# Kernel tuning notes

Hardware: AMD Instinct MI355X
Metric: run time of the kernel (lower is better)

The kernel has to match this reference:

```python
import jax, jax.numpy as jnp
import numpy as np

B, T, C = 8, 2048, 1024
HEAD = 128
ROPE_BASE = 10000.0


def _rope_cos_sin(T, head_dim, base=ROPE_BASE):
    half = head_dim // 2
    inv_freq = base ** (-jnp.arange(half, dtype=jnp.float32) / half)  # (half,)
    t = jnp.arange(T, dtype=jnp.float32)[:, None]                    # (T,1)
    freqs = t * inv_freq[None, :]                                    # (T, half)
    return jnp.cos(freqs), jnp.sin(freqs)


def apply_rope(x, cos, sin):
    # x: (B,T,D), cos/sin: (T,D/2); pairwise (interleaved) rotation
    x_even = x[..., ::2]
    x_odd = x[..., 1::2]
    c = cos[None]
    s = sin[None]
    r_even = x_even * c - x_odd * s
    r_odd = x_even * s + x_odd * c
    # interleave back: (..., D/2, 2) -> (..., D)
    return jnp.stack([r_even, r_odd], axis=-1).reshape(x.shape)


def setup_inputs() -> dict:
    key = jax.random.key(0)
    kx, kk, kq, kv = jax.random.split(key, 4)
    x = jax.random.normal(kx, (B, T, C), dtype=jnp.float32)
    # nn.Linear default init scale ~ 1/sqrt(fan_in); keep activations sane
    scale = 1.0 / np.sqrt(C)
    Wk = jax.random.normal(kk, (C, HEAD), dtype=jnp.float32) * scale
    Wq = jax.random.normal(kq, (C, HEAD), dtype=jnp.float32) * scale
    Wv = jax.random.normal(kv, (C, HEAD), dtype=jnp.float32) * scale
    cos, sin = _rope_cos_sin(T, HEAD)
    return {"x": x, "cos": cos, "sin": sin, "Wk": Wk, "Wq": Wq, "Wv": Wv}


def reference(x, cos, sin, Wk, Wq, Wv):
    # QKV projections (no bias, per nn.Linear(..., bias=False))
    k = jnp.einsum('btc,cd->btd', x, Wk)
    q = jnp.einsum('btc,cd->btd', x, Wq)
    v = jnp.einsum('btc,cd->btd', x, Wv)
    q = apply_rope(q, cos, sin)
    k = apply_rope(k, cos, sin)
    d = k.shape[-1]
    wei = jnp.einsum('bqd,bkd->bqk', q, k) / jnp.sqrt(jnp.asarray(d, q.dtype))
    t = x.shape[1]
    causal = jnp.tril(jnp.ones((t, t), dtype=bool))
    wei = jnp.where(causal[None], wei, jnp.asarray(-jnp.inf, wei.dtype))
    wei = jax.nn.softmax(wei, axis=-1)
    # dropout is identity in eval/reference mode
    out = jnp.einsum('bqk,bkd->bqd', wei, v)
    return out
```

## Files before the change

### kernel.cpp

```cpp
#include <hip/hip_runtime.h>

#define B_ 8
#define T_ 2048
#define C_ 1024
#define D_ 128
#define M_ (B_*T_)

typedef __attribute__((ext_vector_type(4))) float f32x4;
typedef __attribute__((ext_vector_type(8))) short s16x8;

static __device__ __forceinline__ ushort f2bf(float f){
  unsigned u = __float_as_uint(f);
  u = (u + 0x7fffu + ((u >> 16) & 1u)) >> 16;
  return (ushort)u;
}
static __device__ __forceinline__ float bf2f(ushort u){
  return __uint_as_float(((unsigned)u) << 16);
}
static __device__ __forceinline__ unsigned cvt_pk_bf16(float lo, float hi){
  unsigned r;
  asm volatile("v_cvt_pk_bf16_f32 %0, %1, %2" : "=v"(r) : "v"(lo), "v"(hi));
  return r;
}

__global__ __launch_bounds__(256) void prep_kernel(
    const float* __restrict__ x,
    const float* __restrict__ Wk, const float* __restrict__ Wq, const float* __restrict__ Wv,
    ushort* __restrict__ xbf, ushort* __restrict__ wt)
{
  int bid = blockIdx.x, tid = threadIdx.x;
  if (bid < 8192) {
    int idx = bid * 256 + tid;
    const float4* xp = (const float4*)x;
    float4 a = xp[idx * 2], b = xp[idx * 2 + 1];
    uint4 st;
    st.x = (unsigned)f2bf(a.x) | ((unsigned)f2bf(a.y) << 16);
    st.y = (unsigned)f2bf(a.z) | ((unsigned)f2bf(a.w) << 16);
    st.z = (unsigned)f2bf(b.x) | ((unsigned)f2bf(b.y) << 16);
    st.w = (unsigned)f2bf(b.z) | ((unsigned)f2bf(b.w) << 16);
    ((uint4*)xbf)[idx] = st;
  } else {
    int j = (bid - 8192) * 256 + tid;
    if (j < 384 * 1024) {
      int n3 = j >> 10, k = j & 1023;
      int sel = n3 >> 7, n = n3 & 127;
      const float* W = (sel == 0) ? Wq : (sel == 1) ? Wk : Wv;
      wt[j] = f2bf(W[k * 128 + n]);
    }
  }
}

__global__ __launch_bounds__(512) void qkv_kernel(
    const ushort* __restrict__ xbf, const ushort* __restrict__ wt,
    const float* __restrict__ cosp, const float* __restrict__ sinp,
    ushort* __restrict__ Qw, ushort* __restrict__ Kw, ushort* __restrict__ VT)
{
  __shared__ __align__(16) ushort As[2][64 * 64];
  __shared__ __align__(16) ushort Bs[2][384 * 64];
  const int tid = threadIdx.x;
  const int m0  = blockIdx.x * 64;
  const int wid = tid >> 6, lane = tid & 63;
  const int wm = wid >> 2, wn = wid & 3;
  const int g = lane >> 4, l15 = lane & 15;

  f32x4 acc[2][6];
  #pragma unroll
  for (int i = 0; i < 2; i++)
    #pragma unroll
    for (int j = 0; j < 6; j++) acc[i][j] = f32x4{0.f, 0.f, 0.f, 0.f};

  const int o = tid * 16;
  const int srow = o >> 7;
  const int scb  = (o & 127) ^ ((srow & 7) << 4);
  const char* xbase = (const char*)xbf + (size_t)(m0 + srow) * 2048 + scb;
  const char* wbase = (const char*)wt + (size_t)srow * 2048 + scb;

  auto stage = [&](int k0, int bb) {
    __builtin_amdgcn_global_load_lds(
        (const __attribute__((address_space(1))) void*)(xbase + k0 * 2),
        (__attribute__((address_space(3))) void*)((char*)As + bb * 8192 + o), 16, 0, 0);
    #pragma unroll
    for (int j = 0; j < 6; j++) {
      __builtin_amdgcn_global_load_lds(
          (const __attribute__((address_space(1))) void*)(wbase + (size_t)j * 64 * 2048 + k0 * 2),
          (__attribute__((address_space(3))) void*)((char*)Bs + bb * 49152 + j * 8192 + o), 16, 0, 0);
    }
  };

  stage(0, 0);
  __syncthreads();
  int bb = 0;
  for (int k0 = 0; k0 < 1024; k0 += 64) {
    if (k0 + 64 < 1024) stage(k0 + 64, bb ^ 1);
    const char* Ab = (const char*)As + bb * 8192;
    const char* Bb = (const char*)Bs + bb * 49152;
    #pragma unroll
    for (int kk = 0; kk < 2; kk++) {
      s16x8 af[2];
      #pragma unroll
      for (int mi = 0; mi < 2; mi++) {
        int row = wm * 32 + mi * 16 + l15;
        int cb  = (kk * 64 + g * 16) ^ ((row & 7) << 4);
        af[mi] = *(const s16x8*)(Ab + row * 128 + cb);
      }
      s16x8 bfr[6];
      #pragma unroll
      for (int n = 0; n < 6; n++) {
        int col = wn * 96 + n * 16 + l15;
        int cb2 = (kk * 64 + g * 16) ^ ((col & 7) << 4);
        bfr[n] = *(const s16x8*)(Bb + col * 128 + cb2);
      }
      __builtin_amdgcn_s_setprio(1);
      #pragma unroll
      for (int mi = 0; mi < 2; mi++)
        #pragma unroll
        for (int n = 0; n < 6; n++)
          acc[mi][n] = __builtin_amdgcn_mfma_f32_16x16x32_bf16(af[mi], bfr[n], acc[mi][n], 0, 0, 0);
      __builtin_amdgcn_s_setprio(0);
    }
    __syncthreads();
    bb ^= 1;
  }

  const int rowb0 = m0 + wm * 32;
  #pragma unroll
  for (int mi = 0; mi < 2; mi++) {
    #pragma unroll
    for (int n = 0; n < 6; n++) {
      int colbase = wn * 96 + n * 16;
      int region  = colbase >> 7;
      int dcol    = (colbase & 127) + l15;
      int rowb    = rowb0 + mi * 16 + g * 4;
      if (region < 2) {
        ushort* dst = region ? Kw : Qw;
        int ii = dcol >> 1;
        float sgn = (dcol & 1) ? 1.0f : -1.0f;
        #pragma unroll
        for (int r = 0; r < 4; r++) {
          float own  = acc[mi][n][r];
          float part = __shfl_xor(own, 1, 64);
          int row = rowb + r;
          int t   = row & 2047;
          float c = cosp[t * 64 + ii], s = sinp[t * 64 + ii];
          float val = own * c + sgn * part * s;
          dst[row * 128 + dcol] = f2bf(val);
        }
      } else {
        int t0 = rowb & 2047;
        int b  = rowb >> 11;
        unsigned w0 = (unsigned)f2bf(acc[mi][n][0]) | ((unsigned)f2bf(acc[mi][n][1]) << 16);
        unsigned w1 = (unsigned)f2bf(acc[mi][n][2]) | ((unsigned)f2bf(acc[mi][n][3]) << 16);
        uint2 st; st.x = w0; st.y = w1;
        *(uint2*)(VT + (size_t)b * (128 * 2048) + dcol * 2048 + t0) = st;
      }
    }
  }
}

__global__ __launch_bounds__(256) void attn_kernel(
    const ushort* __restrict__ Qw, const ushort* __restrict__ Kw,
    const ushort* __restrict__ VT, ushort* __restrict__ Opart,
    float* __restrict__ Ml)
{
  __shared__ __align__(16) ushort KVs[2][16384];
  const int tid = threadIdx.x;
  const int w = tid >> 6, lane = tid & 63;
  const int g = lane >> 4, l15 = lane & 15;

  const int bid = blockIdx.x;
  const int b   = bid / 144;
  const int idx = bid - b * 144;
  int a = 0;
  #pragma unroll
  for (int t = 1; t < 8; t++) if (idx >= 2 * t * (t + 1)) a = t;
  const int rem = idx - 2 * a * (a + 1);
  const int jin = rem / (a + 1);
  const int c   = rem - jin * (a + 1);
  const int j   = a * 4 + jin;
  const int q0  = j * 64;
  const int kv_base = c * 256;
  const int kv_end  = min(kv_base + 256, q0 + 64);
  const int nt  = (kv_end - kv_base) >> 6;
  const int qg  = q0 + w * 16 + l15;

  const ushort* Qb = Qw + (size_t)b * T_ * 128;
  const char* Kbase = (const char*)(Kw + (size_t)b * T_ * 128);
  const char* Vbase = (const char*)(VT + (size_t)b * 128 * T_);

  auto stage = [&](int kv0, int bbuf) {
    char* Kd = (char*)&KVs[bbuf][0];
    char* Vd = (char*)&KVs[bbuf][8192];
    #pragma unroll
    for (int p = 0; p < 4; p++) {
      int oo = p * 4096 + tid * 16;
      int r = oo >> 8, cin = oo & 255;
      int cb = cin ^ ((r & 7) << 4);
      __builtin_amdgcn_global_load_lds(
          (const __attribute__((address_space(1))) void*)(Kbase + (size_t)(kv0 + r) * 256 + cb),
          (__attribute__((address_space(3))) void*)(Kd + oo), 16, 0, 0);
    }
    #pragma unroll
    for (int p = 0; p < 4; p++) {
      int oo = p * 4096 + tid * 16;
      int r = oo >> 7, cin = oo & 127;
      int cb = cin ^ ((r & 7) << 4);
      __builtin_amdgcn_global_load_lds(
          (const __attribute__((address_space(1))) void*)(Vbase + (size_t)r * 4096 + (size_t)kv0 * 2 + cb),
          (__attribute__((address_space(3))) void*)(Vd + oo), 16, 0, 0);
    }
  };

  s16x8 qf[4];
  #pragma unroll
  for (int kd = 0; kd < 4; kd++)
    qf[kd] = *(const s16x8*)(Qb + qg * 128 + kd * 32 + g * 8);

  f32x4 acco[8];
  #pragma unroll
  for (int i = 0; i < 8; i++) acco[i] = f32x4{0.f, 0.f, 0.f, 0.f};
  float mrun = -1e30f, lrun = 0.0f;
  const float scale = 0.08838834764831845f;

  stage(kv_base, 0);
  __syncthreads();
  int bbuf = 0;
  for (int t = 0; t < nt; t++) {
    int kv0 = kv_base + t * 64;
    if (t + 1 < nt) stage(kv0 + 64, bbuf ^ 1);
    const char* Kd = (const char*)&KVs[bbuf][0];
    const char* Vd = (const char*)&KVs[bbuf][8192];

    f32x4 accs[4];
    #pragma unroll
    for (int h = 0; h < 4; h++) accs[h] = f32x4{0.f, 0.f, 0.f, 0.f};
    __builtin_amdgcn_s_setprio(1);
    #pragma unroll
    for (int h = 0; h < 4; h++) {
      int rr = h * 16 + l15;
      int rs = rr * 256;
      int sw = (rr & 7) << 4;
      #pragma unroll
      for (int kd = 0; kd < 4; kd++) {
        s16x8 kf = *(const s16x8*)(Kd + rs + ((kd * 64 + g * 16) ^ sw));
        accs[h] = __builtin_amdgcn_mfma_f32_16x16x32_bf16(kf, qf[kd], accs[h], 0, 0, 0);
      }
    }
    __builtin_amdgcn_s_setprio(0);

    float p[4][4];
    float pmax = -1e30f;
    #pragma unroll
    for (int h = 0; h < 4; h++)
      #pragma unroll
      for (int r = 0; r < 4; r++) {
        int kvg = kv0 + h * 16 + g * 4 + r;
        float sv = accs[h][r] * scale;
        sv = (kvg <= qg) ? sv : -1e30f;
        p[h][r] = sv;
        pmax = fmaxf(pmax, sv);
      }
    pmax = fmaxf(pmax, __shfl_xor(pmax, 16, 64));
    pmax = fmaxf(pmax, __shfl_xor(pmax, 32, 64));
    float mnew = fmaxf(mrun, pmax);
    float f = __expf(mrun - mnew);
    float psum = 0.0f;
    #pragma unroll
    for (int h = 0; h < 4; h++)
      #pragma unroll
      for (int r = 0; r < 4; r++) { float e = __expf(p[h][r] - mnew); p[h][r] = e; psum += e; }
    psum += __shfl_xor(psum, 16, 64);
    psum += __shfl_xor(psum, 32, 64);
    lrun = lrun * f + psum;
    mrun = mnew;
    #pragma unroll
    for (int i = 0; i < 8; i++) acco[i] *= f;

    unsigned pbw[2][4];
    #pragma unroll
    for (int hk = 0; hk < 2; hk++) {
      unsigned v0 = cvt_pk_bf16(p[2 * hk][0], p[2 * hk][1]);
      unsigned v1 = cvt_pk_bf16(p[2 * hk][2], p[2 * hk][3]);
      unsigned v2 = cvt_pk_bf16(p[2 * hk + 1][0], p[2 * hk + 1][1]);
      unsigned v3 = cvt_pk_bf16(p[2 * hk + 1][2], p[2 * hk + 1][3]);
      #pragma unroll
      for (int wd = 0; wd < 4; wd++) {
        int src = (((g & 1) * 2 + (wd >> 1)) << 4) + l15;
        unsigned t0 = __shfl((wd & 1) ? v1 : v0, src, 64);
        unsigned t1 = __shfl((wd & 1) ? v3 : v2, src, 64);
        pbw[hk][wd] = (g < 2) ? t0 : t1;
      }
    }
    s16x8 pbv0 = *(s16x8*)pbw[0];
    s16x8 pbv1 = *(s16x8*)pbw[1];

    __builtin_amdgcn_s_setprio(1);
    #pragma unroll
    for (int dt = 0; dt < 8; dt++) {
      int rr = dt * 16 + l15;
      int rs = rr * 128;
      int sw = (rr & 7) << 4;
      s16x8 vf0 = *(const s16x8*)(Vd + rs + ((g * 16) ^ sw));
      s16x8 vf1 = *(const s16x8*)(Vd + rs + ((64 + g * 16) ^ sw));
      acco[dt] = __builtin_amdgcn_mfma_f32_16x16x32_bf16(vf0, pbv0, acco[dt], 0, 0, 0);
      acco[dt] = __builtin_amdgcn_mfma_f32_16x16x32_bf16(vf1, pbv1, acco[dt], 0, 0, 0);
    }
    __builtin_amdgcn_s_setprio(0);
    __syncthreads();
    bbuf ^= 1;
  }

  float inv = 1.0f / lrun;
  ushort* ob = Opart + (size_t)bid * 8192 + (w * 16 + l15) * 128;
  #pragma unroll
  for (int dt = 0; dt < 8; dt++) {
    f32x4 o4 = acco[dt] * inv;
    uint2 st;
    st.x = cvt_pk_bf16(o4[0], o4[1]);
    st.y = cvt_pk_bf16(o4[2], o4[3]);
    *(uint2*)(ob + dt * 16 + g * 4) = st;
  }
  if (lane < 16) {
    Ml[(size_t)bid * 128 + (w * 16 + lane) * 2]     = mrun;
    Ml[(size_t)bid * 128 + (w * 16 + lane) * 2 + 1] = lrun;
  }
}

__global__ __launch_bounds__(512) void combine_kernel(
    const ushort* __restrict__ Opart, const float* __restrict__ Ml,
    float* __restrict__ out)
{
  const int bq = blockIdx.x;
  const int b = bq >> 5, j = bq & 31;
  const int a = j >> 2, jin = j & 3, nch = a + 1;
  const int s0 = b * 144 + 2 * a * (a + 1) + jin * (a + 1);
  const int tid = threadIdx.x;
  const int row = tid >> 3, ci = tid & 7;

  float M = -1e30f;
  for (int c = 0; c < nch; c++)
    M = fmaxf(M, Ml[(size_t)(s0 + c) * 128 + row * 2]);

  float acc[16];
  #pragma unroll
  for (int k = 0; k < 16; k++) acc[k] = 0.f;
  float W = 0.f;
  for (int c = 0; c < nch; c++) {
    float m = Ml[(size_t)(s0 + c) * 128 + row * 2];
    float l = Ml[(size_t)(s0 + c) * 128 + row * 2 + 1];
    float wgt = l * __expf(m - M);
    W += wgt;
    const ushort* vp = Opart + (size_t)(s0 + c) * 8192 + row * 128 + ci * 16;
    s16x8 v0 = *(const s16x8*)vp;
    s16x8 v1 = *(const s16x8*)(vp + 8);
    #pragma unroll
    for (int k = 0; k < 8; k++) {
      acc[k]     += wgt * bf2f((ushort)v0[k]);
      acc[8 + k] += wgt * bf2f((ushort)v1[k]);
    }
  }
  float invW = 1.0f / W;
  float* op = out + ((size_t)(b * 2048 + j * 64 + row)) * 128 + ci * 16;
  #pragma unroll
  for (int q = 0; q < 4; q++) {
    f32x4 o4 { acc[q*4]*invW, acc[q*4+1]*invW, acc[q*4+2]*invW, acc[q*4+3]*invW };
    *(f32x4*)(op + q * 4) = o4;
  }
}

extern "C" void kernel_launch(void* const* d_in, const int* in_sizes, int n_in,
                              void* d_out, int out_size, void* d_ws, size_t ws_size,
                              hipStream_t stream)
{
  const float* x    = (const float*)d_in[0];
  const float* cosp = (const float*)d_in[1];
  const float* sinp = (const float*)d_in[2];
  const float* Wk   = (const float*)d_in[3];
  const float* Wq   = (const float*)d_in[4];
  const float* Wv   = (const float*)d_in[5];
  char* ws = (char*)d_ws;
  ushort* xbf   = (ushort*)ws;
  ushort* wt    = (ushort*)(ws + 33554432);
  ushort* Qw    = (ushort*)(ws + 34340864);
  ushort* Kw    = (ushort*)(ws + 38535168);
  ushort* VT    = (ushort*)(ws + 42729472);
  ushort* Opart = (ushort*)ws;
  float*  Ml    = (float*)(ws + 18874368);
  float* outp = (float*)d_out;

  prep_kernel<<<9728, 256, 0, stream>>>(x, Wk, Wq, Wv, xbf, wt);
  qkv_kernel<<<256, 512, 0, stream>>>(xbf, wt, cosp, sinp, Qw, Kw, VT);
  attn_kernel<<<1152, 256, 0, stream>>>(Qw, Kw, VT, Opart, Ml);
  combine_kernel<<<256, 512, 0, stream>>>(Opart, Ml, outp);
}
```

Measured before the change: 175.6 us.

## Fuse x bf16 conversion into QKV GEMM and double attention query tile

Removes the separate full-x fp32-to-bf16 conversion pass: the QKV GEMM now loads fp32 x directly, converts it in registers and writes the bf16 tile into LDS while the B tile streams in asynchronously. The attention kernel now handles 128 query rows per block (two 16-row subtiles per wave), so each K/V tile staged in LDS is reused twice. This halves the number of attention blocks and split partials, at the cost of more registers per wave and possibly lower occupancy. The workspace layout and the combine indexing are updated to match.

Measured after the change: 167.7 us. -4.5%, faster.

```diff
diff --git a/kernel.cpp b/kernel.cpp
--- a/kernel.cpp
+++ b/kernel.cpp
@@ -4,7 +4,6 @@
 #define T_ 2048
 #define C_ 1024
 #define D_ 128
-#define M_ (B_*T_)
 
 typedef __attribute__((ext_vector_type(4))) float f32x4;
 typedef __attribute__((ext_vector_type(8))) short s16x8;
@@ -23,35 +22,19 @@
   return r;
 }
 
-__global__ __launch_bounds__(256) void prep_kernel(
-    const float* __restrict__ x,
+__global__ __launch_bounds__(256) void wprep_kernel(
     const float* __restrict__ Wk, const float* __restrict__ Wq, const float* __restrict__ Wv,
-    ushort* __restrict__ xbf, ushort* __restrict__ wt)
+    ushort* __restrict__ wt)
 {
-  int bid = blockIdx.x, tid = threadIdx.x;
-  if (bid < 8192) {
-    int idx = bid * 256 + tid;
-    const float4* xp = (const float4*)x;
-    float4 a = xp[idx * 2], b = xp[idx * 2 + 1];
-    uint4 st;
-    st.x = (unsigned)f2bf(a.x) | ((unsigned)f2bf(a.y) << 16);
-    st.y = (unsigned)f2bf(a.z) | ((unsigned)f2bf(a.w) << 16);
-    st.z = (unsigned)f2bf(b.x) | ((unsigned)f2bf(b.y) << 16);
-    st.w = (unsigned)f2bf(b.z) | ((unsigned)f2bf(b.w) << 16);
-    ((uint4*)xbf)[idx] = st;
-  } else {
-    int j = (bid - 8192) * 256 + tid;
-    if (j < 384 * 1024) {
-      int n3 = j >> 10, k = j & 1023;
-      int sel = n3 >> 7, n = n3 & 127;
-      const float* W = (sel == 0) ? Wq : (sel == 1) ? Wk : Wv;
-      wt[j] = f2bf(W[k * 128 + n]);
-    }
-  }
+  int j = blockIdx.x * 256 + threadIdx.x;
+  int n3 = j >> 10, k = j & 1023;
+  int sel = n3 >> 7, n = n3 & 127;
+  const float* W = (sel == 0) ? Wq : (sel == 1) ? Wk : Wv;
+  wt[j] = f2bf(W[k * 128 + n]);
 }
 
 __global__ __launch_bounds__(512) void qkv_kernel(
-    const ushort* __restrict__ xbf, const ushort* __restrict__ wt,
+    const float* __restrict__ x, const ushort* __restrict__ wt,
     const float* __restrict__ cosp, const float* __restrict__ sinp,
     ushort* __restrict__ Qw, ushort* __restrict__ Kw, ushort* __restrict__ VT)
 {
@@ -72,13 +55,13 @@
   const int o = tid * 16;
   const int srow = o >> 7;
   const int scb  = (o & 127) ^ ((srow & 7) << 4);
-  const char* xbase = (const char*)xbf + (size_t)(m0 + srow) * 2048 + scb;
   const char* wbase = (const char*)wt + (size_t)srow * 2048 + scb;
-
-  auto stage = [&](int k0, int bb) {
-    __builtin_amdgcn_global_load_lds(
-        (const __attribute__((address_space(1))) void*)(xbase + k0 * 2),
-        (__attribute__((address_space(3))) void*)((char*)As + bb * 8192 + o), 16, 0, 0);
+  const int arow = tid >> 3;
+  const int ac8  = (tid & 7) * 8;
+  const float* xp = x + (size_t)(m0 + arow) * 1024 + ac8;
+  const int adst = arow * 64 + (((tid & 7) * 8) ^ ((arow & 7) << 3));
+
+  auto stageB = [&](int k0, int bb) {
     #pragma unroll
     for (int j = 0; j < 6; j++) {
       __builtin_amdgcn_global_load_lds(
@@ -86,12 +69,29 @@
           (__attribute__((address_space(3))) void*)((char*)Bs + bb * 49152 + j * 8192 + o), 16, 0, 0);
     }
   };
-
-  stage(0, 0);
+  auto writeA = [&](f32x4 a0, f32x4 a1, int bb) {
+    unsigned aw[4];
+    aw[0] = cvt_pk_bf16(a0[0], a0[1]);
+    aw[1] = cvt_pk_bf16(a0[2], a0[3]);
+    aw[2] = cvt_pk_bf16(a1[0], a1[1]);
+    aw[3] = cvt_pk_bf16(a1[2], a1[3]);
+    *(s16x8*)(&As[bb][adst]) = *(s16x8*)aw;
+  };
+
+  {
+    f32x4 a0 = *(const f32x4*)(xp);
+    f32x4 a1 = *(const f32x4*)(xp + 4);
+    stageB(0, 0);
+    writeA(a0, a1, 0);
+  }
   __syncthreads();
   int bb = 0;
   for (int k0 = 0; k0 < 1024; k0 += 64) {
-    if (k0 + 64 < 1024) stage(k0 + 64, bb ^ 1);
+    int k1 = (k0 + 64 < 1024) ? k0 + 64 : 0;
+    f32x4 n0 = *(const f32x4*)(xp + k1);
+    f32x4 n1 = *(const f32x4*)(xp + k1 + 4);
+    stageB(k1, bb ^ 1);
+
     const char* Ab = (const char*)As + bb * 8192;
     const char* Bb = (const char*)Bs + bb * 49152;
     #pragma unroll
@@ -118,6 +118,7 @@
           acc[mi][n] = __builtin_amdgcn_mfma_f32_16x16x32_bf16(af[mi], bfr[n], acc[mi][n], 0, 0, 0);
       __builtin_amdgcn_s_setprio(0);
     }
+    writeA(n0, n1, bb ^ 1);
     __syncthreads();
     bb ^= 1;
   }
@@ -168,20 +169,22 @@
   const int g = lane >> 4, l15 = lane & 15;
 
   const int bid = blockIdx.x;
-  const int b   = bid / 144;
-  const int idx = bid - b * 144;
+  const int b   = bid / 72;
+  const int idx = bid - b * 72;
   int a = 0;
   #pragma unroll
-  for (int t = 1; t < 8; t++) if (idx >= 2 * t * (t + 1)) a = t;
-  const int rem = idx - 2 * a * (a + 1);
+  for (int t = 1; t < 8; t++) if (idx >= t * (t + 1)) a = t;
+  const int rem = idx - a * (a + 1);
   const int jin = rem / (a + 1);
   const int c   = rem - jin * (a + 1);
-  const int j   = a * 4 + jin;
-  const int q0  = j * 64;
+  const int j   = 2 * a + jin;
+  const int q0  = j * 128;
   const int kv_base = c * 256;
-  const int kv_end  = min(kv_base + 256, q0 + 64);
+  const int kv_end  = min(kv_base + 256, q0 + 128);
   const int nt  = (kv_end - kv_base) >> 6;
-  const int qg  = q0 + w * 16 + l15;
+  int qg[2];
+  qg[0] = q0 + w * 32 + l15;
+  qg[1] = qg[0] + 16;
 
   const ushort* Qb = Qw + (size_t)b * T_ * 128;
   const char* Kbase = (const char*)(Kw + (size_t)b * T_ * 128);
@@ -210,15 +213,19 @@
     }
   };
 
-  s16x8 qf[4];
-  #pragma unroll
-  for (int kd = 0; kd < 4; kd++)
-    qf[kd] = *(const s16x8*)(Qb + qg * 128 + kd * 32 + g * 8);
-
-  f32x4 acco[8];
-  #pragma unroll
-  for (int i = 0; i < 8; i++) acco[i] = f32x4{0.f, 0.f, 0.f, 0.f};
-  float mrun = -1e30f, lrun = 0.0f;
+  s16x8 qf[2][4];
+  #pragma unroll
+  for (int i = 0; i < 2; i++)
+    #pragma unroll
+    for (int kd = 0; kd < 4; kd++)
+      qf[i][kd] = *(const s16x8*)(Qb + (size_t)qg[i] * 128 + kd * 32 + g * 8);
+
+  f32x4 acco[2][8];
+  #pragma unroll
+  for (int i = 0; i < 2; i++)
+    #pragma unroll
+    for (int d = 0; d < 8; d++) acco[i][d] = f32x4{0.f, 0.f, 0.f, 0.f};
+  float mrun[2] = {-1e30f, -1e30f}, lrun[2] = {0.f, 0.f};
   const float scale = 0.08838834764831845f;
 
   stage(kv_base, 0);
@@ -230,9 +237,11 @@
     const char* Kd = (const char*)&KVs[bbuf][0];
     const char* Vd = (const char*)&KVs[bbuf][8192];
 
-    f32x4 accs[4];
-    #pragma unroll
-    for (int h = 0; h < 4; h++) accs[h] = f32x4{0.f, 0.f, 0.f, 0.f};
+    f32x4 accs[2][4];
+    #pragma unroll
+    for (int i = 0; i < 2; i++)
+      #pragma unroll
+      for (int h = 0; h < 4; h++) accs[i][h] = f32x4{0.f, 0.f, 0.f, 0.f};
     __builtin_amdgcn_s_setprio(1);
     #pragma unroll
     for (int h = 0; h < 4; h++) {
@@ -242,56 +251,60 @@
       #pragma unroll
       for (int kd = 0; kd < 4; kd++) {
         s16x8 kf = *(const s16x8*)(Kd + rs + ((kd * 64 + g * 16) ^ sw));
-        accs[h] = __builtin_amdgcn_mfma_f32_16x16x32_bf16(kf, qf[kd], accs[h], 0, 0, 0);
+        accs[0][h] = __builtin_amdgcn_mfma_f32_16x16x32_bf16(kf, qf[0][kd], accs[0][h], 0, 0, 0);
+        accs[1][h] = __builtin_amdgcn_mfma_f32_16x16x32_bf16(kf, qf[1][kd], accs[1][h], 0, 0, 0);
       }
     }
     __builtin_amdgcn_s_setprio(0);
 
-    float p[4][4];
-    float pmax = -1e30f;
-    #pragma unroll
-    for (int h = 0; h < 4; h++)
-      #pragma unroll
-      for (int r = 0; r < 4; r++) {
-        int kvg = kv0 + h * 16 + g * 4 + r;
-        float sv = accs[h][r] * scale;
-        sv = (kvg <= qg) ? sv : -1e30f;
-        p[h][r] = sv;
-        pmax = fmaxf(pmax, sv);
+    s16x8 pbv[2][2];
+    #pragma unroll
+    for (int i = 0; i < 2; i++) {
+      float p[4][4];
+      float pmax = -1e30f;
+      #pragma unroll
+      for (int h = 0; h < 4; h++)
+        #pragma unroll
+        for (int r = 0; r < 4; r++) {
+          int kvg = kv0 + h * 16 + g * 4 + r;
+          float sv = accs[i][h][r] * scale;
+          sv = (kvg <= qg[i]) ? sv : -1e30f;
+          p[h][r] = sv;
+          pmax = fmaxf(pmax, sv);
+        }
+      pmax = fmaxf(pmax, __shfl_xor(pmax, 16, 64));
+      pmax = fmaxf(pmax, __shfl_xor(pmax, 32, 64));
+      float mnew = fmaxf(mrun[i], pmax);
+      float f = __expf(mrun[i] - mnew);
+      float psum = 0.0f;
+      #pragma unroll
+      for (int h = 0; h < 4; h++)
+        #pragma unroll
+        for (int r = 0; r < 4; r++) { float e = __expf(p[h][r] - mnew); p[h][r] = e; psum += e; }
+      psum += __shfl_xor(psum, 16, 64);
+      psum += __shfl_xor(psum, 32, 64);
+      lrun[i] = lrun[i] * f + psum;
+      mrun[i] = mnew;
+      #pragma unroll
+      for (int d = 0; d < 8; d++) acco[i][d] *= f;
+
+      #pragma unroll
+      for (int hk = 0; hk < 2; hk++) {
+        unsigned v0 = cvt_pk_bf16(p[2 * hk][0], p[2 * hk][1]);
+        unsigned v1 = cvt_pk_bf16(p[2 * hk][2], p[2 * hk][3]);
+        unsigned v2 = cvt_pk_bf16(p[2 * hk + 1][0], p[2 * hk + 1][1]);
+        unsigned v3 = cvt_pk_bf16(p[2 * hk + 1][2], p[2 * hk + 1][3]);
+        unsigned pb[4];
+        #pragma unroll
+        for (int wd = 0; wd < 4; wd++) {
+          int src = (((g & 1) * 2 + (wd >> 1)) << 4) + l15;
+          unsigned t0 = __shfl((wd & 1) ? v1 : v0, src, 64);
+          unsigned t1 = __shfl((wd & 1) ? v3 : v2, src, 64);
+          pb[wd] = (g < 2) ? t0 : t1;
+        }
+        pbv[i][hk] = *(s16x8*)pb;
       }
-    pmax = fmaxf(pmax, __shfl_xor(pmax, 16, 64));
-    pmax = fmaxf(pmax, __shfl_xor(pmax, 32, 64));
-    float mnew = fmaxf(mrun, pmax);
-    float f = __expf(mrun - mnew);
-    float psum = 0.0f;
-    #pragma unroll
-    for (int h = 0; h < 4; h++)
-      #pragma unroll
-      for (int r = 0; r < 4; r++) { float e = __expf(p[h][r] - mnew); p[h][r] = e; psum += e; }
-    psum += __shfl_xor(psum, 16, 64);
-    psum += __shfl_xor(psum, 32, 64);
-    lrun = lrun * f + psum;
-    mrun = mnew;
-    #pragma unroll
-    for (int i = 0; i < 8; i++) acco[i] *= f;
-
-    unsigned pbw[2][4];
-    #pragma unroll
-    for (int hk = 0; hk < 2; hk++) {
-      unsigned v0 = cvt_pk_bf16(p[2 * hk][0], p[2 * hk][1]);
-      unsigned v1 = cvt_pk_bf16(p[2 * hk][2], p[2 * hk][3]);
-      unsigned v2 = cvt_pk_bf16(p[2 * hk + 1][0], p[2 * hk + 1][1]);
-      unsigned v3 = cvt_pk_bf16(p[2 * hk + 1][2], p[2 * hk + 1][3]);
-      #pragma unroll
-      for (int wd = 0; wd < 4; wd++) {
-        int src = (((g & 1) * 2 + (wd >> 1)) << 4) + l15;
-        unsigned t0 = __shfl((wd & 1) ? v1 : v0, src, 64);
-        unsigned t1 = __shfl((wd & 1) ? v3 : v2, src, 64);
-        pbw[hk][wd] = (g < 2) ? t0 : t1;
-      }
-    }
-    s16x8 pbv0 = *(s16x8*)pbw[0];
-    s16x8 pbv1 = *(s16x8*)pbw[1];
+    }
 
     __builtin_amdgcn_s_setprio(1);
     #pragma unroll
@@ -301,27 +314,32 @@
       int sw = (rr & 7) << 4;
       s16x8 vf0 = *(const s16x8*)(Vd + rs + ((g * 16) ^ sw));
       s16x8 vf1 = *(const s16x8*)(Vd + rs + ((64 + g * 16) ^ sw));
-      acco[dt] = __builtin_amdgcn_mfma_f32_16x16x32_bf16(vf0, pbv0, acco[dt], 0, 0, 0);
-      acco[dt] = __builtin_amdgcn_mfma_f32_16x16x32_bf16(vf1, pbv1, acco[dt], 0, 0, 0);
+      acco[0][dt] = __builtin_amdgcn_mfma_f32_16x16x32_bf16(vf0, pbv[0][0], acco[0][dt], 0, 0, 0);
+      acco[0][dt] = __builtin_amdgcn_mfma_f32_16x16x32_bf16(vf1, pbv[0][1], acco[0][dt], 0, 0, 0);
+      acco[1][dt] = __builtin_amdgcn_mfma_f32_16x16x32_bf16(vf0, pbv[1][0], acco[1][dt], 0, 0, 0);
+      acco[1][dt] = __builtin_amdgcn_mfma_f32_16x16x32_bf16(vf1, pbv[1][1], acco[1][dt], 0, 0, 0);
     }
     __builtin_amdgcn_s_setprio(0);
     __syncthreads();
     bbuf ^= 1;
   }
 
-  float inv = 1.0f / lrun;
-  ushort* ob = Opart + (size_t)bid * 8192 + (w * 16 + l15) * 128;
-  #pragma unroll
-  for (int dt = 0; dt < 8; dt++) {
-    f32x4 o4 = acco[dt] * inv;
-    uint2 st;
-    st.x = cvt_pk_bf16(o4[0], o4[1]);
-    st.y = cvt_pk_bf16(o4[2], o4[3]);
-    *(uint2*)(ob + dt * 16 + g * 4) = st;
-  }
-  if (lane < 16) {
-    Ml[(size_t)bid * 128 + (w * 16 + lane) * 2]     = mrun;
-    Ml[(size_t)bid * 128 + (w * 16 + lane) * 2 + 1] = lrun;
+  #pragma unroll
+  for (int i = 0; i < 2; i++) {
+    float inv = 1.0f / lrun[i];
+    ushort* ob = Opart + (size_t)bid * 16384 + (w * 32 + i * 16 + l15) * 128;
+    #pragma unroll
+    for (int dt = 0; dt < 8; dt++) {
+      f32x4 o4 = acco[i][dt] * inv;
+      uint2 st;
+      st.x = cvt_pk_bf16(o4[0], o4[1]);
+      st.y = cvt_pk_bf16(o4[2], o4[3]);
+      *(uint2*)(ob + dt * 16 + g * 4) = st;
+    }
+    if (lane < 16) {
+      Ml[(size_t)bid * 256 + (w * 32 + i * 16 + lane) * 2]     = mrun[i];
+      Ml[(size_t)bid * 256 + (w * 32 + i * 16 + lane) * 2 + 1] = lrun[i];
+    }
   }
 }
 
@@ -330,26 +348,27 @@
     float* __restrict__ out)
 {
   const int bq = blockIdx.x;
-  const int b = bq >> 5, j = bq & 31;
-  const int a = j >> 2, jin = j & 3, nch = a + 1;
-  const int s0 = b * 144 + 2 * a * (a + 1) + jin * (a + 1);
+  const int b = bq >> 5, h = bq & 31;
+  const int j = h >> 1, half = h & 1;
+  const int a = j >> 1, jin = j & 1, nch = a + 1;
+  const int s0 = b * 72 + a * (a + 1) + jin * (a + 1);
   const int tid = threadIdx.x;
-  const int row = tid >> 3, ci = tid & 7;
+  const int row = half * 64 + (tid >> 3), ci = tid & 7;
 
   float M = -1e30f;
   for (int c = 0; c < nch; c++)
-    M = fmaxf(M, Ml[(size_t)(s0 + c) * 128 + row * 2]);
+    M = fmaxf(M, Ml[(size_t)(s0 + c) * 256 + row * 2]);
 
   float acc[16];
   #pragma unroll
   for (int k = 0; k < 16; k++) acc[k] = 0.f;
   float W = 0.f;
   for (int c = 0; c < nch; c++) {
-    float m = Ml[(size_t)(s0 + c) * 128 + row * 2];
-    float l = Ml[(size_t)(s0 + c) * 128 + row * 2 + 1];
+    float m = Ml[(size_t)(s0 + c) * 256 + row * 2];
+    float l = Ml[(size_t)(s0 + c) * 256 + row * 2 + 1];
     float wgt = l * __expf(m - M);
     W += wgt;
-    const ushort* vp = Opart + (size_t)(s0 + c) * 8192 + row * 128 + ci * 16;
+    const ushort* vp = Opart + (size_t)(s0 + c) * 16384 + row * 128 + ci * 16;
     s16x8 v0 = *(const s16x8*)vp;
     s16x8 v1 = *(const s16x8*)(vp + 8);
     #pragma unroll
@@ -359,7 +378,7 @@
     }
   }
   float invW = 1.0f / W;
-  float* op = out + ((size_t)(b * 2048 + j * 64 + row)) * 128 + ci * 16;
+  float* op = out + ((size_t)(b * 2048 + h * 64 + (tid >> 3))) * 128 + ci * 16;
   #pragma unroll
   for (int q = 0; q < 4; q++) {
     f32x4 o4 { acc[q*4]*invW, acc[q*4+1]*invW, acc[q*4+2]*invW, acc[q*4+3]*invW };
@@ -378,17 +397,16 @@
   const float* Wq   = (const float*)d_in[4];
   const float* Wv   = (const float*)d_in[5];
   char* ws = (char*)d_ws;
-  ushort* xbf   = (ushort*)ws;
-  ushort* wt    = (ushort*)(ws + 33554432);
-  ushort* Qw    = (ushort*)(ws + 34340864);
-  ushort* Kw    = (ushort*)(ws + 38535168);
-  ushort* VT    = (ushort*)(ws + 42729472);
-  ushort* Opart = (ushort*)ws;
-  float*  Ml    = (float*)(ws + 18874368);
+  ushort* wt    = (ushort*)ws;
+  ushort* Qw    = (ushort*)(ws + 1048576);
+  ushort* Kw    = (ushort*)(ws + 5242880);
+  ushort* VT    = (ushort*)(ws + 9437184);
+  ushort* Opart = (ushort*)(ws + 13631488);
+  float*  Ml    = (float*)(ws + 32505856);
   float* outp = (float*)d_out;
 
-  prep_kernel<<<9728, 256, 0, stream>>>(x, Wk, Wq, Wv, xbf, wt);
-  qkv_kernel<<<256, 512, 0, stream>>>(xbf, wt, cosp, sinp, Qw, Kw, VT);
-  attn_kernel<<<1152, 256, 0, stream>>>(Qw, Kw, VT, Opart, Ml);
+  wprep_kernel<<<1536, 256, 0, stream>>>(Wk, Wq, Wv, wt);
+  qkv_kernel<<<256, 512, 0, stream>>>(x, wt, cosp, sinp, Qw, Kw, VT);
+  attn_kernel<<<576, 256, 0, stream>>>(Qw, Kw, VT, Opart, Ml);
   combine_kernel<<<256, 512, 0, stream>>>(Opart, Ml, outp);
 }
```
